# Kernel optimization log

Measured on AMD Instinct MI355X. Metric: run time of the kernel, lower is better.

## Reference

```python
import jax, jax.numpy as jnp
import numpy as np

B, COND_LEN, E = 128, 256, 512   # batch, cond_len, hidden_dim (== conditioning_dim)
A, L, H = 128, 64, 8             # action_dim, num_action_steps, num_heads
STEPS = 20
HD = E // H


def setup_inputs() -> dict:
    key = jax.random.key(0)
    ks = jax.random.split(key, 16)
    def rn(k, shape, s=0.02):
        return jax.random.normal(k, shape, jnp.float32) * s
    return {
        "conditioning": jax.random.normal(ks[0], (B, COND_LEN, E), jnp.float32),
        "noise": jax.random.normal(ks[1], (B, L, A), jnp.float32),
        # time_embed: Linear(1,E) -> ReLU -> Linear(E,E)
        "t1_w": rn(ks[2], (E, 1)), "t1_b": jnp.zeros((E,), jnp.float32),
        "t2_w": rn(ks[3], (E, E)), "t2_b": jnp.zeros((E,), jnp.float32),
        # query_proj: Linear(A, E)
        "qp_w": rn(ks[4], (E, A)), "qp_b": jnp.zeros((E,), jnp.float32),
        # MultiheadAttention packed in_proj (3E, E) and out_proj (E, E)
        "in_w": rn(ks[5], (3 * E, E)), "in_b": jnp.zeros((3 * E,), jnp.float32),
        "op_w": rn(ks[6], (E, E)), "op_b": jnp.zeros((E,), jnp.float32),
        # output_proj: Linear(E, A)
        "outp_w": rn(ks[7], (A, E)), "outp_b": jnp.zeros((A,), jnp.float32),
        # ffn: Linear(A, 4A) -> ReLU -> Linear(4A, A)
        "f1_w": rn(ks[8], (4 * A, A)), "f1_b": jnp.zeros((4 * A,), jnp.float32),
        "f2_w": rn(ks[9], (A, 4 * A)), "f2_b": jnp.zeros((A,), jnp.float32),
        # LayerNorm(A)
        "ln_g": jnp.ones((A,), jnp.float32), "ln_b": jnp.zeros((A,), jnp.float32),
    }


def reference(conditioning, noise, t1_w, t1_b, t2_w, t2_b, qp_w, qp_b,
              in_w, in_b, op_w, op_b, outp_w, outp_b,
              f1_w, f1_b, f2_w, f2_b, ln_g, ln_b):
    dt = -1.0 / STEPS
    scale = 1.0 / np.sqrt(HD)
    # K/V of cross-attn depend only on conditioning -> hoist out of the loop
    # (same math as recomputing per step).
    k = (conditioning @ in_w[E:2 * E].T + in_b[E:2 * E]).reshape(B, COND_LEN, H, HD)
    v = (conditioning @ in_w[2 * E:].T + in_b[2 * E:]).reshape(B, COND_LEN, H, HD)

    def denoise(x_t, time):
        t = time[:, None]                                            # (B,1)
        t_emb = jnp.maximum(t @ t1_w.T + t1_b, 0.0) @ t2_w.T + t2_b  # (B,E)
        q_in = x_t @ qp_w.T + qp_b + t_emb[:, None, :]               # (B,L,E)
        q = (q_in @ in_w[:E].T + in_b[:E]).reshape(B, L, H, HD)
        scores = jnp.einsum('bqhd,bkhd->bhqk', q * scale, k)         # (B,H,L,COND_LEN)
        attn = jax.nn.softmax(scores, axis=-1)
        ctx = jnp.einsum('bhqk,bkhd->bqhd', attn, v).reshape(B, L, E)
        ctx = ctx @ op_w.T + op_b                                    # MHA out_proj
        v_t = ctx @ outp_w.T + outp_b                                # (B,L,A)
        h = x_t + v_t
        mu = jnp.mean(h, axis=-1, keepdims=True)
        var = jnp.mean((h - mu) ** 2, axis=-1, keepdims=True)
        hn = (h - mu) / jnp.sqrt(var + 1e-5) * ln_g + ln_b
        return hn + (jnp.maximum(hn @ f1_w.T + f1_b, 0.0) @ f2_w.T + f2_b)

    def step(carry, _):
        x_t, time = carry
        v_t = denoise(x_t, time)
        return (x_t + dt * v_t, time + dt), None

    init = (noise, jnp.ones((B,), jnp.float32))
    (x_t, _), _ = jax.lax.scan(step, init, None, length=STEPS)
    return x_t
```

## Files before the change

kernel.cpp:

```cpp
#include <hip/hip_runtime.h>

#define NB 128
#define CL 256
#define EE 512
#define AA 128
#define LL 64
#define HH 8
#define HD 64
#define NSTEPS 20
#define BLROWS (NB*LL)
#define LOG2E 1.4426950408889634f
#define QSCALE 64.0f
#define INV_QS 0.015625f

typedef __attribute__((ext_vector_type(8))) short bf16x8;
typedef __attribute__((ext_vector_type(4))) float f32x4;
typedef unsigned int u32;

union F8 { u32 u[2]; long l; };

__device__ __forceinline__ unsigned short f2bf(float f) {
    union { float f; unsigned u; } x; x.f = f;
    unsigned u = x.u;
    u += 0x7fffu + ((u >> 16) & 1u);
    return (unsigned short)(u >> 16);
}
__device__ __forceinline__ u32 pk4f8(f32x4 v) {
    u32 r = __builtin_amdgcn_cvt_pk_fp8_f32(v[0], v[1], 0, false);
    r = __builtin_amdgcn_cvt_pk_fp8_f32(v[2], v[3], r, true);
    return r;
}
__device__ __forceinline__ unsigned char f2f8(float v) {
    return (unsigned char)(__builtin_amdgcn_cvt_pk_fp8_f32(v, v, 0, false) & 0xffu);
}

__device__ __forceinline__ void async_copy16(const unsigned short* g, unsigned short* l) {
    __builtin_amdgcn_global_load_lds((const __attribute__((address_space(1))) u32*)g,
                                     (__attribute__((address_space(3))) u32*)l, 16, 0, 0);
}

#define MFMA(a,b,c)  __builtin_amdgcn_mfma_f32_16x16x32_bf16(a, b, c, 0, 0, 0)
#define MFMA8(a,b,c) __builtin_amdgcn_mfma_f32_16x16x32_fp8_fp8(a, b, c, 0, 0, 0)

__device__ __forceinline__ F8 build8(const u32* p, int kk, int srcA, int srcB, int odd) {
    u32 a0 = __shfl((int)p[2*kk],   srcA, 64);
    u32 b0 = __shfl((int)p[2*kk+1], srcA, 64);
    u32 a1 = __shfl((int)p[2*kk],   srcB, 64);
    u32 b1 = __shfl((int)p[2*kk+1], srcB, 64);
    F8 f; f.u[0] = odd ? b0 : a0; f.u[1] = odd ? b1 : a1;
    return f;
}

__device__ __forceinline__ void softmax8(f32x4* sacc, u32* pp8) {
    float mx0 = sacc[0][0], mx1 = sacc[0][1], mx2 = sacc[0][2], mx3 = sacc[0][3];
#pragma unroll
    for (int t = 1; t < 16; ++t) {
        mx0 = fmaxf(mx0, sacc[t][0]);
        mx1 = fmaxf(mx1, sacc[t][1]);
        mx2 = fmaxf(mx2, sacc[t][2]);
        mx3 = fmaxf(mx3, sacc[t][3]);
    }
    float mx = fmaxf(fmaxf(mx0, mx1), fmaxf(mx2, mx3));
    mx = fmaxf(mx, __shfl_xor(mx, 16));
    mx = fmaxf(mx, __shfl_xor(mx, 32));
    float mxc = mx * INV_QS;
    float s0 = 0.f, s1 = 0.f, s2 = 0.f, s3 = 0.f;
#pragma unroll
    for (int t = 0; t < 16; ++t) {
        float e0 = exp2f(fmaf(sacc[t][0], INV_QS, -mxc));
        float e1 = exp2f(fmaf(sacc[t][1], INV_QS, -mxc));
        float e2 = exp2f(fmaf(sacc[t][2], INV_QS, -mxc));
        float e3 = exp2f(fmaf(sacc[t][3], INV_QS, -mxc));
        sacc[t][0] = e0; sacc[t][1] = e1; sacc[t][2] = e2; sacc[t][3] = e3;
        s0 += e0; s1 += e1; s2 += e2; s3 += e3;
    }
    float sum = (s0 + s1) + (s2 + s3);
    sum += __shfl_xor(sum, 16);
    sum += __shfl_xor(sum, 32);
    float iv = QSCALE / sum;
#pragma unroll
    for (int t = 0; t < 16; ++t) {
        f32x4 w = sacc[t];
        w[0]*=iv; w[1]*=iv; w[2]*=iv; w[3]*=iv;
        pp8[t] = pk4f8(w);
    }
}


__global__ void cvt8_kernel(const float* __restrict__ src, unsigned short* __restrict__ dst, int n8) {
    int i = blockIdx.x*256 + threadIdx.x;
    if (i >= n8) return;
    const float* s = src + (size_t)i*8;
    f32x4 v0 = *(const f32x4*)s;
    f32x4 v1 = *(const f32x4*)(s + 4);
    bf16x8 o;
    o[0]=(short)f2bf(v0[0]); o[1]=(short)f2bf(v0[1]);
    o[2]=(short)f2bf(v0[2]); o[3]=(short)f2bf(v0[3]);
    o[4]=(short)f2bf(v1[0]); o[5]=(short)f2bf(v1[1]);
    o[6]=(short)f2bf(v1[2]); o[7]=(short)f2bf(v1[3]);
    *(bf16x8*)(dst + (size_t)i*8) = o;
}

__global__ void prep_eff_kernel(const float* __restrict__ in_w, const float* __restrict__ qp_w,
                                const float* __restrict__ outp_w, const float* __restrict__ op_w,
                                const float* __restrict__ op_b, const float* __restrict__ outp_b,
                                unsigned short* __restrict__ wq, unsigned short* __restrict__ wo,
                                float* __restrict__ bo) {
    int tid = blockIdx.x*256 + threadIdx.x;
    if (tid < 65536) {
        int n = tid >> 7, k = tid & 127;
        float s = 0.f;
        for (int e = 0; e < 512; ++e) s += in_w[(size_t)n*512 + e] * qp_w[(size_t)e*128 + k];
        wq[(size_t)n*128 + k] = f2bf(s * (0.125f * LOG2E * QSCALE));
    } else if (tid < 131072) {
        int t2 = tid - 65536; int n = t2 >> 9, k = t2 & 511;
        float s = 0.f;
        for (int e = 0; e < 512; ++e) s += outp_w[(size_t)n*512 + e] * op_w[(size_t)e*512 + k];
        wo[(size_t)n*512 + k] = f2bf(s);
    } else if (tid < 131200) {
        int n = tid - 131072;
        float s = outp_b[n];
        for (int e = 0; e < 512; ++e) s += outp_w[(size_t)n*512 + e] * op_b[e];
        bo[n] = s;
    }
}

__global__ void temb_kernel(const float* __restrict__ t1_w, const float* __restrict__ t1_b,
                            const float* __restrict__ t2_w, const float* __restrict__ t2_b,
                            float* __restrict__ temb) {
    int tid = blockIdx.x*256 + threadIdx.x;
    if (tid >= NSTEPS*512) return;
    int s = tid >> 9, e = tid & 511;
    float t = 1.0f - 0.05f * (float)s;
    float acc = t2_b[e];
    for (int i = 0; i < 512; ++i)
        acc += t2_w[(size_t)e*512 + i] * fmaxf(t * t1_w[i] + t1_b[i], 0.f);
    temb[tid] = acc;
}

__global__ void qbias_kernel(const float* __restrict__ in_w, const float* __restrict__ in_b,
                             const float* __restrict__ qp_b, const float* __restrict__ temb,
                             float* __restrict__ qbias) {
    int tid = blockIdx.x*256 + threadIdx.x;
    if (tid >= NSTEPS*512) return;
    int s = tid >> 9, n = tid & 511;
    float acc = in_b[n];
    const float* te = temb + (size_t)s*512;
    for (int e = 0; e < 512; ++e)
        acc += in_w[(size_t)n*512 + e] * (qp_b[e] + te[e]);
    qbias[tid] = acc * (0.125f * LOG2E * QSCALE);
}

__global__ __launch_bounds__(512, 8) void kv_kernel(const unsigned short* __restrict__ condb,
                                                    const unsigned short* __restrict__ wkv,
                                                    const float* __restrict__ bias,
                                                    unsigned char* __restrict__ K8,
                                                    unsigned char* __restrict__ V8) {
    __shared__ unsigned short As[128*64];
    __shared__ unsigned short Bs[128*64];
    int tid = threadIdx.x;
    int blk = blockIdx.x;
    int xcd = blk & 7, j = blk >> 3;
    int m0 = (xcd*32 + (j >> 3)) * 128;
    int n0 = (j & 7) * 128;
    int wv = tid >> 6, lane = tid & 63, r = lane & 15, q = lane >> 4;
    int srow = lane >> 3;
    int sg = (lane & 7) ^ srow;
    const unsigned short* agl = condb + (size_t)(m0 + wv*16 + srow)*512 + sg*8;
    const unsigned short* bgl = wkv   + (size_t)(n0 + wv*16 + srow)*512 + sg*8;
    f32x4 acc[8] = {};
#pragma unroll
    for (int kt = 0; kt < 8; ++kt) {
        int k0 = kt * 64;
#pragma unroll
        for (int ii = 0; ii < 2; ++ii) {
            async_copy16(agl + (size_t)(ii*8)*512 + k0, &As[(wv*16 + ii*8)*64]);
            async_copy16(bgl + (size_t)(ii*8)*512 + k0, &Bs[(wv*16 + ii*8)*64]);
        }
        __syncthreads();
#pragma unroll
        for (int kk = 0; kk < 2; ++kk) {
            int gof = ((kk*4 + q) ^ (r & 7)) * 8;
            bf16x8 a = *(const bf16x8*)&As[(wv*16 + r)*64 + gof];
#pragma unroll
            for (int t = 0; t < 8; ++t) {
                bf16x8 b = *(const bf16x8*)&Bs[(t*16 + r)*64 + gof];
                acc[t] = MFMA(a, b, acc[t]);
            }
        }
        __syncthreads();
    }
    int mbase = m0 + wv*16 + q*4;
    int bb = mbase >> 8, kpb = mbase & 255;
#pragma unroll
    for (int t = 0; t < 8; ++t) {
        int n = n0 + t*16 + r;
        float bs = bias[n];
        if (n < 512) {
            int h = n >> 6, d = n & 63;
            int colp = ((d>>3)&3)*16 + ((d>>5)&1)*8 + (d&7);
            unsigned char* kp = K8 + (size_t)(bb*HH + h)*16384 + colp;
#pragma unroll
            for (int i = 0; i < 4; ++i)
                kp[(kpb + i)*64] = f2f8(acc[t][i] + bs);
        } else {
            int n2 = n - 512, h = n2 >> 6, d = n2 & 63;
            int kk = kpb >> 5, qq = (kpb >> 3) & 3, jb = kpb & 7;
            int colv = (kk>>1)*64 + qq*16 + (kk&1)*8 + jb;
            u32 w01 = __builtin_amdgcn_cvt_pk_fp8_f32(acc[t][0]+bs, acc[t][1]+bs, 0, false);
            w01 = __builtin_amdgcn_cvt_pk_fp8_f32(acc[t][2]+bs, acc[t][3]+bs, w01, true);
            *(u32*)(V8 + (size_t)(bb*HH + h)*16384 + d*256 + colv) = w01;
        }
    }
}

__global__ __launch_bounds__(512, 2) void mega_kernel(
        const unsigned char* __restrict__ Kg,
        const unsigned char* __restrict__ Vg,
        const float* __restrict__ noise,
        const unsigned short* __restrict__ wq,
        const float* __restrict__ qbiasB,
        const unsigned short* __restrict__ wo,
        const float* __restrict__ bo,
        const float* __restrict__ ln_g, const float* __restrict__ ln_b,
        const unsigned short* __restrict__ f1w,
        const float* __restrict__ f1_b,
        const unsigned short* __restrict__ f2w,
        const float* __restrict__ f2_b,
        float* __restrict__ outp) {
    __shared__ unsigned short xS[32*136];
    __shared__ unsigned short cuS[32*520];
    __shared__ unsigned short hnS[32*136];
    __shared__ float redS[32*4], redS2[32*4];

    int tid = threadIdx.x, w = tid >> 6, lane = tid & 63, r = lane & 15, q = lane >> 4;
    int vblk = ((blockIdx.x & 7) << 5) | (blockIdx.x >> 3);
    int b = vblk >> 1;
    int row0 = vblk * 32;
    int h = w;
    int tB = w & 1, cg = w >> 1;
    int srcA = r + ((2*q) & 3)*16;
    int srcB = r + ((2*q + 1) & 3)*16;
    int odd = (q >> 1) & 1;

    float xf[2][4];
#pragma unroll
    for (int t = 0; t < 2; ++t)
#pragma unroll
        for (int i = 0; i < 4; ++i) {
            int rl = tB*16 + q*4 + i, col = cg*32 + t*16 + r;
            float v = noise[(size_t)(row0 + rl)*AA + col];
            xf[t][i] = v;
            xS[rl*136 + col] = f2bf(v);
        }

    size_t bh = (size_t)b*HH + h;
    const unsigned char* kbase = Kg + bh*16384;
    const unsigned char* vbase = Vg + bh*16384;
    __syncthreads();

    const float dt = -1.f / (float)NSTEPS;

#pragma unroll 1
    for (int s = 0; s < NSTEPS; ++s) {
        const float* qb_s = qbiasB + (size_t)s*512;

        {
            f32x4 qacc0[4] = {}, qacc1[4] = {};
#pragma unroll
            for (int kk = 0; kk < 4; ++kk) {
                bf16x8 bx0 = *(const bf16x8*)&xS[(r)*136 + kk*32 + q*8];
                bf16x8 bx1 = *(const bf16x8*)&xS[(16 + r)*136 + kk*32 + q*8];
#pragma unroll
                for (int t = 0; t < 4; ++t) {
                    bf16x8 a = *(const bf16x8*)(wq + (size_t)(h*HD + t*16 + r)*AA + kk*32 + q*8);
                    qacc0[t] = MFMA(a, bx0, qacc0[t]);
                    qacc1[t] = MFMA(a, bx1, qacc1[t]);
                }
            }
            u32 qp0[4], qp1[4];
#pragma unroll
            for (int t = 0; t < 4; ++t) {
                f32x4 qb4 = *(const f32x4*)(qb_s + h*HD + t*16 + q*4);
                f32x4 v0, v1;
#pragma unroll
                for (int i = 0; i < 4; ++i) { v0[i] = qacc0[t][i] + qb4[i]; v1[i] = qacc1[t][i] + qb4[i]; }
                qp0[t] = pk4f8(v0);
                qp1[t] = pk4f8(v1);
            }
            F8 bq0[2], bq1[2];
            bq0[0] = build8(qp0, 0, srcA, srcB, odd);
            bq0[1] = build8(qp0, 1, srcA, srcB, odd);
            bq1[0] = build8(qp1, 0, srcA, srcB, odd);
            bq1[1] = build8(qp1, 1, srcA, srcB, odd);

            f32x4 s0[16] = {}, s1[16] = {};
#pragma unroll
            for (int t = 0; t < 16; ++t) {
                uint4 k4 = *(const uint4*)(kbase + (size_t)(t*16 + r)*64 + q*16);
                F8 k0, k1;
                k0.u[0] = k4.x; k0.u[1] = k4.y;
                k1.u[0] = k4.z; k1.u[1] = k4.w;
                s0[t] = MFMA8(k0.l, bq0[0].l, s0[t]);
                s0[t] = MFMA8(k1.l, bq0[1].l, s0[t]);
                s1[t] = MFMA8(k0.l, bq1[0].l, s1[t]);
                s1[t] = MFMA8(k1.l, bq1[1].l, s1[t]);
            }
            u32 pp0[16], pp1[16];
            softmax8(s0, pp0);
            softmax8(s1, pp1);

            f32x4 c0[4] = {}, c1[4] = {};
#pragma unroll
            for (int kp = 0; kp < 4; ++kp) {
                F8 a00 = build8(pp0, 2*kp,   srcA, srcB, odd);
                F8 a01 = build8(pp0, 2*kp+1, srcA, srcB, odd);
                F8 a10 = build8(pp1, 2*kp,   srcA, srcB, odd);
                F8 a11 = build8(pp1, 2*kp+1, srcA, srcB, odd);
#pragma unroll
                for (int t = 0; t < 4; ++t) {
                    uint4 v4 = *(const uint4*)(vbase + (size_t)(t*16 + r)*256 + kp*64 + q*16);
                    F8 v0, v1;
                    v0.u[0] = v4.x; v0.u[1] = v4.y;
                    v1.u[0] = v4.z; v1.u[1] = v4.w;
                    c0[t] = MFMA8(a00.l, v0.l, c0[t]);
                    c0[t] = MFMA8(a01.l, v1.l, c0[t]);
                    c1[t] = MFMA8(a10.l, v0.l, c1[t]);
                    c1[t] = MFMA8(a11.l, v1.l, c1[t]);
                }
            }
#pragma unroll
            for (int t = 0; t < 4; ++t)
#pragma unroll
                for (int i = 0; i < 4; ++i) {
                    cuS[(q*4 + i)*520 + h*HD + t*16 + r]      = f2bf(c0[t][i] * INV_QS);
                    cuS[(16 + q*4 + i)*520 + h*HD + t*16 + r] = f2bf(c1[t][i] * INV_QS);
                }
        }
        __syncthreads();

        f32x4 oacc[2] = {};
#pragma unroll
        for (int kk = 0; kk < 16; ++kk) {
            bf16x8 a = *(const bf16x8*)&cuS[(tB*16 + r)*520 + kk*32 + q*8];
#pragma unroll
            for (int t = 0; t < 2; ++t) {
                bf16x8 bw = *(const bf16x8*)(wo + (size_t)(cg*32 + t*16 + r)*EE + kk*32 + q*8);
                oacc[t] = MFMA(a, bw, oacc[t]);
            }
        }
        float hv[2][4];
#pragma unroll
        for (int t = 0; t < 2; ++t) {
            float bov = bo[cg*32 + t*16 + r];
#pragma unroll
            for (int i = 0; i < 4; ++i) hv[t][i] = oacc[t][i] + bov + xf[t][i];
        }
#pragma unroll
        for (int i = 0; i < 4; ++i) {
            float s1 = hv[0][i] + hv[1][i];
            float s2 = hv[0][i]*hv[0][i] + hv[1][i]*hv[1][i];
            s1 += __shfl_xor(s1, 1);  s2 += __shfl_xor(s2, 1);
            s1 += __shfl_xor(s1, 2);  s2 += __shfl_xor(s2, 2);
            s1 += __shfl_xor(s1, 4);  s2 += __shfl_xor(s2, 4);
            s1 += __shfl_xor(s1, 8);  s2 += __shfl_xor(s2, 8);
            if (r == 0) { redS[(tB*16 + q*4 + i)*4 + cg] = s1; redS2[(tB*16 + q*4 + i)*4 + cg] = s2; }
        }
        __syncthreads();
        float hnv[2][4];
#pragma unroll
        for (int i = 0; i < 4; ++i) {
            int row = tB*16 + q*4 + i;
            float s1 = redS [row*4+0] + redS [row*4+1] + redS [row*4+2] + redS [row*4+3];
            float s2 = redS2[row*4+0] + redS2[row*4+1] + redS2[row*4+2] + redS2[row*4+3];
            float mu = s1 * (1.f/128.f);
            float var = s2 * (1.f/128.f) - mu*mu;
            float rstd = rsqrtf(var + 1e-5f);
#pragma unroll
            for (int t = 0; t < 2; ++t) {
                int col = cg*32 + t*16 + r;
                float v = (hv[t][i] - mu) * rstd * ln_g[col] + ln_b[col];
                hnv[t][i] = v;
                hnS[row*136 + col] = f2bf(v);
            }
        }
        __syncthreads();

        f32x4 o2[2] = {};
#pragma unroll 1
        for (int nt = 0; nt < 4; ++nt) {
            f32x4 a1[2] = {};
#pragma unroll
            for (int kk = 0; kk < 4; ++kk) {
                bf16x8 a = *(const bf16x8*)&hnS[(tB*16 + r)*136 + kk*32 + q*8];
#pragma unroll
                for (int t = 0; t < 2; ++t) {
                    bf16x8 bw = *(const bf16x8*)(f1w + (size_t)(nt*128 + cg*32 + t*16 + r)*AA + kk*32 + q*8);
                    a1[t] = MFMA(a, bw, a1[t]);
                }
            }
#pragma unroll
            for (int t = 0; t < 2; ++t) {
                float b1 = f1_b[nt*128 + cg*32 + t*16 + r];
#pragma unroll
                for (int i = 0; i < 4; ++i)
                    cuS[(tB*16 + q*4 + i)*520 + nt*128 + cg*32 + t*16 + r] = f2bf(fmaxf(a1[t][i] + b1, 0.f));
            }
        }
        __syncthreads();
#pragma unroll 1
        for (int nt = 0; nt < 4; ++nt) {
#pragma unroll
            for (int kk = 0; kk < 4; ++kk) {
                bf16x8 a = *(const bf16x8*)&cuS[(tB*16 + r)*520 + nt*128 + kk*32 + q*8];
#pragma unroll
                for (int t = 0; t < 2; ++t) {
                    bf16x8 bw = *(const bf16x8*)(f2w + (size_t)(cg*32 + t*16 + r)*EE + nt*128 + kk*32 + q*8);
                    o2[t] = MFMA(a, bw, o2[t]);
                }
            }
        }

        if (s < NSTEPS - 1) {
#pragma unroll
            for (int t = 0; t < 2; ++t) {
                float b2 = f2_b[cg*32 + t*16 + r];
#pragma unroll
                for (int i = 0; i < 4; ++i) {
                    float outv = hnv[t][i] + o2[t][i] + b2;
                    float xn = xf[t][i] + dt * outv;
                    xf[t][i] = xn;
                    xS[(tB*16 + q*4 + i)*136 + cg*32 + t*16 + r] = f2bf(xn);
                }
            }
            __syncthreads();
        } else {
#pragma unroll
            for (int t = 0; t < 2; ++t) {
                float b2 = f2_b[cg*32 + t*16 + r];
#pragma unroll
                for (int i = 0; i < 4; ++i) {
                    float outv = hnv[t][i] + o2[t][i] + b2;
                    outp[(size_t)(row0 + tB*16 + q*4 + i)*AA + cg*32 + t*16 + r] = xf[t][i] + dt * outv;
                }
            }
        }
    }
}

extern "C" void kernel_launch(void* const* d_in, const int* in_sizes, int n_in,
                              void* d_out, int out_size, void* d_ws, size_t ws_size,
                              hipStream_t stream) {
    const float* cond   = (const float*)d_in[0];
    const float* noise  = (const float*)d_in[1];
    const float* t1_w   = (const float*)d_in[2];
    const float* t1_b   = (const float*)d_in[3];
    const float* t2_w   = (const float*)d_in[4];
    const float* t2_b   = (const float*)d_in[5];
    const float* qp_w   = (const float*)d_in[6];
    const float* qp_b   = (const float*)d_in[7];
    const float* in_w   = (const float*)d_in[8];
    const float* in_b   = (const float*)d_in[9];
    const float* op_w   = (const float*)d_in[10];
    const float* op_b   = (const float*)d_in[11];
    const float* outp_w = (const float*)d_in[12];
    const float* outp_b = (const float*)d_in[13];
    const float* f1_w   = (const float*)d_in[14];
    const float* f1_b   = (const float*)d_in[15];
    const float* f2_w   = (const float*)d_in[16];
    const float* f2_b   = (const float*)d_in[17];
    const float* ln_g   = (const float*)d_in[18];
    const float* ln_bp  = (const float*)d_in[19];

    char* w = (char*)d_ws;
    auto alloc = [&](size_t bytes) {
        char* p = w;
        w += (bytes + 255) & ~(size_t)255;
        return p;
    };
    unsigned char*  K8     = (unsigned char*)alloc((size_t)NB*HH*CL*HD);
    unsigned char*  V8     = (unsigned char*)alloc((size_t)NB*HH*HD*CL);
    unsigned short* condb  = (unsigned short*)alloc((size_t)NB*CL*EE*2);
    unsigned short* wkv_bf = (unsigned short*)alloc((size_t)1024*512*2);
    unsigned short* wq_bf  = (unsigned short*)alloc((size_t)512*128*2);
    unsigned short* wo_bf  = (unsigned short*)alloc((size_t)128*512*2);
    unsigned short* f1_bf  = (unsigned short*)alloc((size_t)512*128*2);
    unsigned short* f2_bf  = (unsigned short*)alloc((size_t)128*512*2);
    float*          bo_eff = (float*)alloc(128*4);
    float*          tembB  = (float*)alloc((size_t)NSTEPS*512*4);
    float*          qbiasB = (float*)alloc((size_t)NSTEPS*512*4);
    (void)ws_size; (void)n_in; (void)in_sizes; (void)out_size;

    cvt8_kernel<<<8192, 256, 0, stream>>>(cond, condb, NB*CL*EE/8);
    cvt8_kernel<<<256, 256, 0, stream>>>(in_w + 512*512, wkv_bf, 1024*512/8);
    cvt8_kernel<<<32, 256, 0, stream>>>(f1_w, f1_bf, 512*128/8);
    cvt8_kernel<<<32, 256, 0, stream>>>(f2_w, f2_bf, 128*512/8);
    prep_eff_kernel<<<513, 256, 0, stream>>>(in_w, qp_w, outp_w, op_w, op_b, outp_b,
                                             wq_bf, wo_bf, bo_eff);
    temb_kernel<<<40, 256, 0, stream>>>(t1_w, t1_b, t2_w, t2_b, tembB);
    qbias_kernel<<<40, 256, 0, stream>>>(in_w, in_b, qp_b, tembB, qbiasB);
    kv_kernel<<<2048, 512, 0, stream>>>(condb, wkv_bf, in_b + 512, K8, V8);

    mega_kernel<<<256, 512, 0, stream>>>(K8, V8, noise, wq_bf, qbiasB,
                                         wo_bf, bo_eff, ln_g, ln_bp,
                                         f1_bf, f1_b, f2_bf, f2_b,
                                         (float*)d_out);
}
```

Measured before the change: 1.372 ms.

## Prefetch K/V fp8 tiles into registers and defer softmax normalization

Loads all K tiles into registers before the Q projection and all V tiles before the softmax, so global-memory latency overlaps with MFMA and softmax work. The softmax no longer normalizes probabilities before fp8 packing. It packs exp values scaled by a constant and applies 1/sum per query row to the context output via shuffles. This removes a full pass over the score registers, but it raises register pressure (32 extra uint4) and changes the fp8 quantization range of the unnormalized probabilities.

```diff
diff --git a/kernel.cpp b/kernel.cpp
--- a/kernel.cpp
+++ b/kernel.cpp
@@ -51,7 +51,7 @@
     return f;
 }
 
-__device__ __forceinline__ void softmax8(f32x4* sacc, u32* pp8) {
+__device__ __forceinline__ float softmax8v(const f32x4* sacc, u32* pp8) {
     float mx0 = sacc[0][0], mx1 = sacc[0][1], mx2 = sacc[0][2], mx3 = sacc[0][3];
 #pragma unroll
     for (int t = 1; t < 16; ++t) {
@@ -71,19 +71,16 @@
         float e1 = exp2f(fmaf(sacc[t][1], INV_QS, -mxc));
         float e2 = exp2f(fmaf(sacc[t][2], INV_QS, -mxc));
         float e3 = exp2f(fmaf(sacc[t][3], INV_QS, -mxc));
-        sacc[t][0] = e0; sacc[t][1] = e1; sacc[t][2] = e2; sacc[t][3] = e3;
         s0 += e0; s1 += e1; s2 += e2; s3 += e3;
+        f32x4 w;
+        w[0] = e0 * QSCALE; w[1] = e1 * QSCALE;
+        w[2] = e2 * QSCALE; w[3] = e3 * QSCALE;
+        pp8[t] = pk4f8(w);
     }
     float sum = (s0 + s1) + (s2 + s3);
     sum += __shfl_xor(sum, 16);
     sum += __shfl_xor(sum, 32);
-    float iv = QSCALE / sum;
-#pragma unroll
-    for (int t = 0; t < 16; ++t) {
-        f32x4 w = sacc[t];
-        w[0]*=iv; w[1]*=iv; w[2]*=iv; w[3]*=iv;
-        pp8[t] = pk4f8(w);
-    }
+    return 1.0f / sum;
 }
 
 
@@ -266,6 +263,11 @@
         const float* qb_s = qbiasB + (size_t)s*512;
 
         {
+            uint4 kbuf[16];
+#pragma unroll
+            for (int t = 0; t < 16; ++t)
+                kbuf[t] = *(const uint4*)(kbase + (size_t)(t*16 + r)*64 + q*16);
+
             f32x4 qacc0[4] = {}, qacc1[4] = {};
 #pragma unroll
             for (int kk = 0; kk < 4; ++kk) {
@@ -297,18 +299,25 @@
             f32x4 s0[16] = {}, s1[16] = {};
 #pragma unroll
             for (int t = 0; t < 16; ++t) {
-                uint4 k4 = *(const uint4*)(kbase + (size_t)(t*16 + r)*64 + q*16);
                 F8 k0, k1;
-                k0.u[0] = k4.x; k0.u[1] = k4.y;
-                k1.u[0] = k4.z; k1.u[1] = k4.w;
+                k0.u[0] = kbuf[t].x; k0.u[1] = kbuf[t].y;
+                k1.u[0] = kbuf[t].z; k1.u[1] = kbuf[t].w;
                 s0[t] = MFMA8(k0.l, bq0[0].l, s0[t]);
                 s0[t] = MFMA8(k1.l, bq0[1].l, s0[t]);
                 s1[t] = MFMA8(k0.l, bq1[0].l, s1[t]);
                 s1[t] = MFMA8(k1.l, bq1[1].l, s1[t]);
             }
+
+            uint4 vbuf[16];
+#pragma unroll
+            for (int kp = 0; kp < 4; ++kp)
+#pragma unroll
+                for (int t = 0; t < 4; ++t)
+                    vbuf[kp*4 + t] = *(const uint4*)(vbase + (size_t)(t*16 + r)*256 + kp*64 + q*16);
+
             u32 pp0[16], pp1[16];
-            softmax8(s0, pp0);
-            softmax8(s1, pp1);
+            float iv0 = softmax8v(s0, pp0);
+            float iv1 = softmax8v(s1, pp1);
 
             f32x4 c0[4] = {}, c1[4] = {};
 #pragma unroll
@@ -319,22 +328,27 @@
                 F8 a11 = build8(pp1, 2*kp+1, srcA, srcB, odd);
 #pragma unroll
                 for (int t = 0; t < 4; ++t) {
-                    uint4 v4 = *(const uint4*)(vbase + (size_t)(t*16 + r)*256 + kp*64 + q*16);
                     F8 v0, v1;
-                    v0.u[0] = v4.x; v0.u[1] = v4.y;
-                    v1.u[0] = v4.z; v1.u[1] = v4.w;
+                    v0.u[0] = vbuf[kp*4+t].x; v0.u[1] = vbuf[kp*4+t].y;
+                    v1.u[0] = vbuf[kp*4+t].z; v1.u[1] = vbuf[kp*4+t].w;
                     c0[t] = MFMA8(a00.l, v0.l, c0[t]);
                     c0[t] = MFMA8(a01.l, v1.l, c0[t]);
                     c1[t] = MFMA8(a10.l, v0.l, c1[t]);
                     c1[t] = MFMA8(a11.l, v1.l, c1[t]);
                 }
             }
+            float sc0[4], sc1[4];
+#pragma unroll
+            for (int i = 0; i < 4; ++i) {
+                sc0[i] = INV_QS * __shfl(iv0, q*4 + i);
+                sc1[i] = INV_QS * __shfl(iv1, q*4 + i);
+            }
 #pragma unroll
             for (int t = 0; t < 4; ++t)
 #pragma unroll
                 for (int i = 0; i < 4; ++i) {
-                    cuS[(q*4 + i)*520 + h*HD + t*16 + r]      = f2bf(c0[t][i] * INV_QS);
-                    cuS[(16 + q*4 + i)*520 + h*HD + t*16 + r] = f2bf(c1[t][i] * INV_QS);
+                    cuS[(q*4 + i)*520 + h*HD + t*16 + r]      = f2bf(c0[t][i] * sc0[i]);
+                    cuS[(16 + q*4 + i)*520 + h*HD + t*16 + r] = f2bf(c1[t][i] * sc1[i]);
                 }
         }
         __syncthreads();
```

Result: no change. 1.369 ms (-0.2%).
